# Kernel optimization log

Hardware: AMD Instinct MI355X
Metric: run time of the kernel (lower is better)

Reference implementation:

```python
import jax, jax.numpy as jnp
import numpy as np

THETA = 10.0      # neuron['theta']
TAU_SR = 10.0     # neuron['tauSr']
TAU_REF = 1.0     # neuron['tauRef']
SCALE_REF = 2.0   # neuron['scaleRef']
TAU_RHO = 1.0     # neuron['tauRho']
SCALE_RHO = 1.0   # neuron['scaleRho']
EPS = 0.01        # kernel truncation epsilon
TS = 1.0          # simulation['Ts']
T_SAMPLE = 256    # time steps == seq_len (forward sets tSample = embed_out.size(1))


def _alpha_kernel(tau, mult):
    # slayerPytorch _calculateAlphaKernel: mult * t/tau * exp(1 - t/tau), truncated
    ker = []
    for t in np.arange(0.0, T_SAMPLE * TS, TS):
        v = mult * t / tau * np.exp(1.0 - t / tau)
        if abs(v) < EPS and t > tau:
            break
        ker.append(v)
    return np.asarray(ker, dtype=np.float32)


def psp(x, srm_kernel):
    # Causal temporal filter: out[t] = Ts * sum_k srm[k] * x[t-k];  x: (B, C, T)
    B, C, T = x.shape
    K = srm_kernel.shape[0]
    lhs = x.reshape(B * C, 1, T)
    rhs = srm_kernel[::-1].reshape(1, 1, K)  # reverse: correlation -> convolution
    out = jax.lax.conv_general_dilated(lhs, rhs, (1,), [(K - 1, 0)])
    return out.reshape(B, C, T) * TS


def _spike_scan(u, ref_kernel):
    # Sequential threshold with refractory feedback (SLAYER getSpikes). u: (B, C, T)
    B, C, T = u.shape
    future = ref_kernel[1:]  # ref_kernel[0] == 0, so spike at t only affects t+1..
    R = future.shape[0]

    def step(r, u_t):
        m = u_t + r[..., 0]                       # membrane incl. past refractory
        s = (m >= THETA).astype(u.dtype)
        r = jnp.concatenate([r[..., 1:], jnp.zeros_like(r[..., :1])], axis=-1)
        r = r + s[..., None] * future             # schedule refractory response
        return r, (s, m)

    r0 = jnp.zeros((B, C, R), u.dtype)
    _, (s, m) = jax.lax.scan(step, r0, jnp.moveaxis(u, -1, 0))
    return jnp.moveaxis(s, 0, -1), jnp.moveaxis(m, 0, -1)


@jax.custom_vjp
def spike(u, ref_kernel):
    return _spike_scan(u, ref_kernel)[0]


def _spike_fwd(u, ref_kernel):
    s, m = _spike_scan(u, ref_kernel)
    return s, (m, ref_kernel)


def _spike_bwd(res, g):
    # SLAYER surrogate gradient: straight-through pdf on post-refractory membrane
    m, ref_kernel = res
    tau = TAU_RHO * THETA
    pdf = (SCALE_RHO / tau) * jnp.exp(-jnp.abs(m - THETA) / tau)
    return g * pdf, jnp.zeros_like(ref_kernel)


spike.defvjp(_spike_fwd, _spike_bwd)


def setup_inputs() -> dict:
    key = jax.random.key(0)
    k1, k2, k3, k4 = jax.random.split(key, 4)
    VOCAB, EMB, HID, OUT, B = 50000, 300, 512, 10, 64
    feed_data = jax.random.randint(k1, (B, T_SAMPLE), 0, VOCAB)
    emb_weight = jax.random.normal(k2, (VOCAB, EMB), jnp.float32)
    W1 = jax.random.normal(k3, (HID, EMB), jnp.float32) * (4.0 / np.sqrt(EMB))
    W2 = jax.random.normal(k4, (OUT, HID), jnp.float32) * (4.0 / np.sqrt(HID))
    return {
        "feed_data": feed_data,
        "emb_weight": emb_weight,
        "W1": W1,
        "W2": W2,
        "srm_kernel": jnp.asarray(_alpha_kernel(TAU_SR, 1.0)),
        "ref_kernel": jnp.asarray(_alpha_kernel(TAU_REF, -SCALE_REF * THETA)),
    }


def reference(feed_data, emb_weight, W1, W2, srm_kernel, ref_kernel):
    x = emb_weight[feed_data]                 # (B, T, E); dropout = identity (eval)
    x = jnp.transpose(x, (0, 2, 1))           # (B, E, T) -- transpose(1,2)
    h = jnp.einsum('he,bet->bht', W1, x)      # slayer.dense == 1x1x1 conv3d, no bias
    h = spike(psp(h, srm_kernel), ref_kernel)
    o = jnp.einsum('oh,bht->bot', W2, h)
    return spike(psp(o, srm_kernel), ref_kernel)  # (B, OUT, T)
```

## Files before the change

### kernel.cpp

```cpp
#include <hip/hip_runtime.h>

#define BB    64
#define TT    256
#define EMBD  300
#define HIDD  512
#define OUTC  10
#define THETA 10.0
#define FUTN  12
#define KSMAX 80
#define GT    32
#define GE    8
#define WGRP  9
#define WROW  (64 * WGRP)
#define HSTRD 258

__global__ __launch_bounds__(256)
void w2cvt_kernel(const float* __restrict__ W2, double* __restrict__ w2d)
{
    const int k = blockIdx.x * 256 + threadIdx.x;
    if (k < OUTC * HIDD) w2d[k] = (double)W2[k];
}

__global__ __launch_bounds__(512)
void gemm1_kernel(const int* __restrict__ feed, const float* __restrict__ emb,
                  const float* __restrict__ W1, double* __restrict__ m1)
{
    __shared__ double wl[GE * WROW];
    __shared__ double xs[GE][GT + 1];
    __shared__ int    idxb[GT];

    const int tid = threadIdx.x;
    const int t0  = blockIdx.x * GT;
    const int b   = blockIdx.y;

    if (tid < GT) idxb[tid] = feed[b * TT + t0 + tid];
    __syncthreads();

    const int cg = tid & 63;
    const int tg = tid >> 6;

    double acc[4][8];
#pragma unroll
    for (int i = 0; i < 4; ++i)
#pragma unroll
        for (int j = 0; j < 8; ++j) acc[i][j] = 0.0;

    const int NCH = (EMBD + GE - 1) / GE;
    for (int ch = 0; ch < NCH; ++ch) {
        const int e0 = ch * GE;
        {
            const int c = tid;
            float4 wa = make_float4(0.f, 0.f, 0.f, 0.f);
            float4 wb = make_float4(0.f, 0.f, 0.f, 0.f);
            if (e0 < EMBD)     wa = *(const float4*)&W1[(size_t)c * EMBD + e0];
            if (e0 + 4 < EMBD) wb = *(const float4*)&W1[(size_t)c * EMBD + e0 + 4];
            const int g = (c >> 3) * WGRP + (c & 7);
            wl[0 * WROW + g] = (double)wa.x;
            wl[1 * WROW + g] = (double)wa.y;
            wl[2 * WROW + g] = (double)wa.z;
            wl[3 * WROW + g] = (double)wa.w;
            wl[4 * WROW + g] = (double)wb.x;
            wl[5 * WROW + g] = (double)wb.y;
            wl[6 * WROW + g] = (double)wb.z;
            wl[7 * WROW + g] = (double)wb.w;
        }
        if (tid < 256) {
            const int t = tid >> 3, e = tid & 7;
            const float v = (e0 + e < EMBD)
                ? emb[(size_t)idxb[t] * EMBD + e0 + e] : 0.f;
            xs[e][t] = (double)v;
        }
        __syncthreads();

#pragma unroll
        for (int e = 0; e < GE; ++e) {
            const double* wp = &wl[e * WROW + cg * WGRP];
            const double w0 = wp[0], w1 = wp[1], w2 = wp[2], w3 = wp[3];
            const double w4 = wp[4], w5 = wp[5], w6 = wp[6], w7 = wp[7];
            const double x0 = xs[e][4 * tg + 0];
            const double x1 = xs[e][4 * tg + 1];
            const double x2 = xs[e][4 * tg + 2];
            const double x3 = xs[e][4 * tg + 3];
            acc[0][0] = fma(x0, w0, acc[0][0]); acc[0][1] = fma(x0, w1, acc[0][1]);
            acc[0][2] = fma(x0, w2, acc[0][2]); acc[0][3] = fma(x0, w3, acc[0][3]);
            acc[0][4] = fma(x0, w4, acc[0][4]); acc[0][5] = fma(x0, w5, acc[0][5]);
            acc[0][6] = fma(x0, w6, acc[0][6]); acc[0][7] = fma(x0, w7, acc[0][7]);
            acc[1][0] = fma(x1, w0, acc[1][0]); acc[1][1] = fma(x1, w1, acc[1][1]);
            acc[1][2] = fma(x1, w2, acc[1][2]); acc[1][3] = fma(x1, w3, acc[1][3]);
            acc[1][4] = fma(x1, w4, acc[1][4]); acc[1][5] = fma(x1, w5, acc[1][5]);
            acc[1][6] = fma(x1, w6, acc[1][6]); acc[1][7] = fma(x1, w7, acc[1][7]);
            acc[2][0] = fma(x2, w0, acc[2][0]); acc[2][1] = fma(x2, w1, acc[2][1]);
            acc[2][2] = fma(x2, w2, acc[2][2]); acc[2][3] = fma(x2, w3, acc[2][3]);
            acc[2][4] = fma(x2, w4, acc[2][4]); acc[2][5] = fma(x2, w5, acc[2][5]);
            acc[2][6] = fma(x2, w6, acc[2][6]); acc[2][7] = fma(x2, w7, acc[2][7]);
            acc[3][0] = fma(x3, w0, acc[3][0]); acc[3][1] = fma(x3, w1, acc[3][1]);
            acc[3][2] = fma(x3, w2, acc[3][2]); acc[3][3] = fma(x3, w3, acc[3][3]);
            acc[3][4] = fma(x3, w4, acc[3][4]); acc[3][5] = fma(x3, w5, acc[3][5]);
            acc[3][6] = fma(x3, w6, acc[3][6]); acc[3][7] = fma(x3, w7, acc[3][7]);
        }
        __syncthreads();
    }

#pragma unroll
    for (int i = 0; i < 4; ++i) {
        double* dst = &m1[((size_t)b * TT + t0 + 4 * tg + i) * HIDD + 8 * cg];
        *(double2*)(dst + 0) = make_double2(acc[i][0], acc[i][1]);
        *(double2*)(dst + 2) = make_double2(acc[i][2], acc[i][3]);
        *(double2*)(dst + 4) = make_double2(acc[i][4], acc[i][5]);
        *(double2*)(dst + 6) = make_double2(acc[i][6], acc[i][7]);
    }
}

__global__ __launch_bounds__(256)
void firscan_kernel(const double* __restrict__ m1, const float* __restrict__ srm,
                    const float* __restrict__ refk, unsigned char* __restrict__ s1,
                    int Ks, int Kr)
{
    __shared__ double        h[16 * HSTRD];
    __shared__ unsigned char sb[16 * 260];
    __shared__ double        srm_sm[KSMAX];

    const int tid = threadIdx.x;
    const int c0  = blockIdx.x * 16;
    const int b   = blockIdx.y;

    if (tid < KSMAX) srm_sm[tid] = (tid < Ks) ? (double)srm[tid] : 0.0;

    for (int u = tid; u < 16 * TT; u += 256) {
        const int c = u & 15, t = u >> 4;
        h[c * HSTRD + t] = m1[((size_t)b * TT + t) * HIDD + c0 + c];
    }
    __syncthreads();

    const int cf = tid & 15, tb = tid >> 4;
    const int t0 = tb * 16;
    const double* hrow = &h[cf * HSTRD];

    double pout[16];
#pragma unroll
    for (int k = 0; k < 16; ++k) pout[k] = 0.0;

    double HI[8], MID[8], LO[8];
#pragma unroll
    for (int k = 0; k < 8; ++k) {
        HI[k]  = hrow[t0 + 8 + k];
        MID[k] = hrow[t0 + k];
        const int idx = t0 - 8 + k;
        LO[k] = (idx >= 0) ? hrow[idx] : 0.0;
    }

#pragma unroll
    for (int jb = 0; jb < KSMAX; jb += 8) {
        double NEW[8];
        if (jb + 8 < KSMAX) {
#pragma unroll
            for (int k = 0; k < 8; ++k) {
                const int idx = t0 - jb - 16 + k;
                NEW[k] = (idx >= 0) ? hrow[idx] : 0.0;
            }
        }
#pragma unroll
        for (int jj = 0; jj < 8; ++jj) {
            const double sj = srm_sm[jb + jj];
#pragma unroll
            for (int i = 0; i < 16; ++i) {
                const int d = i - jj;
                const double hv = (d >= 8) ? HI[(d - 8) & 7]
                               : (d >= 0) ? MID[d & 7]
                                          : LO[(8 + d) & 7];
                pout[i] = fma(hv, sj, pout[i]);
            }
        }
        if (jb + 8 < KSMAX) {
#pragma unroll
            for (int k = 0; k < 8; ++k) { HI[k] = MID[k]; MID[k] = LO[k]; LO[k] = NEW[k]; }
        }
    }
    __syncthreads();
#pragma unroll
    for (int k = 0; k < 16; ++k)
        h[cf * HSTRD + t0 + k] = pout[k];
    __syncthreads();

    if (tid < 16) {
        double fut[FUTN], rsh[FUTN];
#pragma unroll
        for (int i = 0; i < FUTN; ++i) {
            fut[i] = (i + 1 < Kr) ? (double)refk[i + 1] : 0.0;
            rsh[i] = 0.0;
        }
        const double*  hr = &h[tid * HSTRD];
        unsigned char* sr = &sb[tid * 260];
        double un = hr[0];
        for (int t = 0; t < TT; ++t) {
            const double uc = un;
            un = (t < TT - 1) ? hr[t + 1] : 0.0;
            const double m  = uc + rsh[0];
            const double sv = (m >= THETA) ? 1.0 : 0.0;
#pragma unroll
            for (int i = 0; i < FUTN - 1; ++i) rsh[i] = fma(sv, fut[i], rsh[i + 1]);
            rsh[FUTN - 1] = sv * fut[FUTN - 1];
            sr[t] = (unsigned char)(sv != 0.0 ? 1 : 0);
        }
    }
    __syncthreads();

    {
        const int tl2 = tid & 63;
#pragma unroll
        for (int r = 0; r < 4; ++r) {
            const int c = (tid >> 6) + 4 * r;
            const unsigned int v = *(const unsigned int*)&sb[c * 260 + 4 * tl2];
            *(unsigned int*)&s1[((size_t)b * HIDD + c0 + c) * TT + 4 * tl2] = v;
        }
    }
}

__global__ __launch_bounds__(256, 2)
void layer2a_kernel(const unsigned char* __restrict__ s1,
                    const double* __restrict__ w2d, double* __restrict__ m2)
{
    __shared__ double w2l[OUTC * HIDD];
    __shared__ double red[4][OUTC][65];

    const int tid = threadIdx.x;
    const int b = blockIdx.x, q = blockIdx.y;
    const int tl = tid & 63, hq = tid >> 6;
    const int t  = q * 64 + tl;

    for (int u = tid; u < OUTC * HIDD; u += 256) w2l[u] = w2d[u];
    __syncthreads();

    double p[OUTC];
#pragma unroll
    for (int oc = 0; oc < OUTC; ++oc) p[oc] = 0.0;

    const unsigned char* sp = s1 + ((size_t)b * HIDD + hq * 128) * TT + t;
    for (int h0 = 0; h0 < 128; ++h0) {
        const double sv = (double)sp[(size_t)h0 * TT];
        const int hh = hq * 128 + h0;
#pragma unroll
        for (int oc = 0; oc < OUTC; ++oc)
            p[oc] = fma(sv, w2l[oc * HIDD + hh], p[oc]);
    }
#pragma unroll
    for (int oc = 0; oc < OUTC; ++oc) red[hq][oc][tl] = p[oc];
    __syncthreads();

    for (int u = tid; u < OUTC * 64; u += 256) {
        const int oc = u >> 6, t2 = u & 63;
        const double s = ((red[0][oc][t2] + red[1][oc][t2]) +
                          red[2][oc][t2]) + red[3][oc][t2];
        m2[((size_t)b * OUTC + oc) * TT + q * 64 + t2] = s;
    }
}

__global__ __launch_bounds__(256)
void layer2b_kernel(const double* __restrict__ m2, const float* __restrict__ srm,
                    const float* __restrict__ refk, float* __restrict__ out,
                    int Ks, int Kr)
{
    __shared__ double mh[OUTC][257];
    __shared__ double uh[OUTC][257];
    __shared__ double srm_sm[KSMAX];
    __shared__ unsigned char s2[OUTC][260];

    const int tid = threadIdx.x;
    const int b   = blockIdx.x;

    if (tid < KSMAX) srm_sm[tid] = (tid < Ks) ? (double)srm[tid] : 0.0;
    for (int u = tid; u < OUTC * TT; u += 256)
        mh[u >> 8][u & 255] = m2[(size_t)b * OUTC * TT + u];
    __syncthreads();

    double p[OUTC];
#pragma unroll
    for (int oc = 0; oc < OUTC; ++oc) p[oc] = 0.0;
    for (int j = 0; j < KSMAX; ++j) {
        const int idx = tid - j;
        if (idx >= 0) {
            const double sj = srm_sm[j];
#pragma unroll
            for (int oc = 0; oc < OUTC; ++oc)
                p[oc] = fma(mh[oc][idx], sj, p[oc]);
        }
    }
#pragma unroll
    for (int oc = 0; oc < OUTC; ++oc) uh[oc][tid] = p[oc];
    __syncthreads();

    if (tid < OUTC) {
        double fut[FUTN], rsh[FUTN];
#pragma unroll
        for (int i = 0; i < FUTN; ++i) {
            fut[i] = (i + 1 < Kr) ? (double)refk[i + 1] : 0.0;
            rsh[i] = 0.0;
        }
        for (int t = 0; t < TT; ++t) {
            const double m  = uh[tid][t] + rsh[0];
            const double sv = (m >= THETA) ? 1.0 : 0.0;
#pragma unroll
            for (int i = 0; i < FUTN - 1; ++i) rsh[i] = fma(sv, fut[i], rsh[i + 1]);
            rsh[FUTN - 1] = sv * fut[FUTN - 1];
            s2[tid][t] = (unsigned char)(sv != 0.0 ? 1 : 0);
        }
    }
    __syncthreads();

    for (int u = tid; u < OUTC * TT; u += 256)
        out[(size_t)b * OUTC * TT + u] = (float)s2[u >> 8][u & 255];
}

extern "C" void kernel_launch(void* const* d_in, const int* in_sizes, int n_in,
                              void* d_out, int out_size, void* d_ws, size_t ws_size,
                              hipStream_t stream)
{
    const int*   feed = (const int*)  d_in[0];
    const float* emb  = (const float*)d_in[1];
    const float* W1   = (const float*)d_in[2];
    const float* W2   = (const float*)d_in[3];
    const float* srm  = (const float*)d_in[4];
    const float* refk = (const float*)d_in[5];
    const int Ks = in_sizes[4];
    const int Kr = in_sizes[5];

    const size_t S1B  = (size_t)BB * HIDD * TT;
    const size_t W2DB = (size_t)OUTC * HIDD * 8;
    const size_t M2B  = (size_t)BB * OUTC * TT * 8;
    unsigned char* s1c = (unsigned char*)d_ws;
    double* w2d = (double*)((char*)d_ws + S1B);
    double* m2  = (double*)((char*)d_ws + S1B + W2DB);
    double* m1  = (double*)((char*)d_ws + S1B + W2DB + M2B);
    float*  out = (float*)d_out;

    w2cvt_kernel  <<<dim3(20),            256, 0, stream>>>(W2, w2d);
    gemm1_kernel  <<<dim3(TT / GT, BB),   512, 0, stream>>>(feed, emb, W1, m1);
    firscan_kernel<<<dim3(HIDD / 16, BB), 256, 0, stream>>>(m1, srm, refk, s1c, Ks, Kr);
    layer2a_kernel<<<dim3(BB, 4),         256, 0, stream>>>(s1c, w2d, m2);
    layer2b_kernel<<<dim3(BB),            256, 0, stream>>>(m2, srm, refk, out, Ks, Kr);
}
```

Before: 443.0 us.

## Split gemm1 across output-channel halves and prefetch next K-chunk into registers

```diff
diff --git a/kernel.cpp b/kernel.cpp
--- a/kernel.cpp
+++ b/kernel.cpp
@@ -9,9 +9,10 @@
 #define FUTN  12
 #define KSMAX 80
 #define GT    32
+#define GC    256
 #define GE    8
 #define WGRP  9
-#define WROW  (64 * WGRP)
+#define WROW  (32 * WGRP)
 #define HSTRD 258
 
 __global__ __launch_bounds__(256)
@@ -21,7 +22,7 @@
     if (k < OUTC * HIDD) w2d[k] = (double)W2[k];
 }
 
-__global__ __launch_bounds__(512)
+__global__ __launch_bounds__(256)
 void gemm1_kernel(const int* __restrict__ feed, const float* __restrict__ emb,
                   const float* __restrict__ W1, double* __restrict__ m1)
 {
@@ -30,14 +31,16 @@
     __shared__ int    idxb[GT];
 
     const int tid = threadIdx.x;
-    const int t0  = blockIdx.x * GT;
+    const int t0  = (blockIdx.x >> 1) * GT;
+    const int c0  = (blockIdx.x & 1) * GC;
     const int b   = blockIdx.y;
 
     if (tid < GT) idxb[tid] = feed[b * TT + t0 + tid];
     __syncthreads();
 
-    const int cg = tid & 63;
-    const int tg = tid >> 6;
+    const int cg = tid & 31;
+    const int tg = tid >> 5;
+    const int xt = tid >> 3, xe = tid & 7;
 
     double acc[4][8];
 #pragma unroll
@@ -45,32 +48,39 @@
 #pragma unroll
         for (int j = 0; j < 8; ++j) acc[i][j] = 0.0;
 
+    const size_t wrow = (size_t)(c0 + tid) * EMBD;
+    const size_t xrow = (size_t)idxb[xt] * EMBD;
+
+    float4 wa = make_float4(0.f, 0.f, 0.f, 0.f);
+    float4 wb = make_float4(0.f, 0.f, 0.f, 0.f);
+    float  xv = 0.f;
+    wa = *(const float4*)&W1[wrow + 0];
+    wb = *(const float4*)&W1[wrow + 4];
+    xv = emb[xrow + xe];
+
     const int NCH = (EMBD + GE - 1) / GE;
+    const int g   = (tid >> 3) * WGRP + (tid & 7);
+
     for (int ch = 0; ch < NCH; ++ch) {
-        const int e0 = ch * GE;
-        {
-            const int c = tid;
-            float4 wa = make_float4(0.f, 0.f, 0.f, 0.f);
-            float4 wb = make_float4(0.f, 0.f, 0.f, 0.f);
-            if (e0 < EMBD)     wa = *(const float4*)&W1[(size_t)c * EMBD + e0];
-            if (e0 + 4 < EMBD) wb = *(const float4*)&W1[(size_t)c * EMBD + e0 + 4];
-            const int g = (c >> 3) * WGRP + (c & 7);
-            wl[0 * WROW + g] = (double)wa.x;
-            wl[1 * WROW + g] = (double)wa.y;
-            wl[2 * WROW + g] = (double)wa.z;
-            wl[3 * WROW + g] = (double)wa.w;
-            wl[4 * WROW + g] = (double)wb.x;
-            wl[5 * WROW + g] = (double)wb.y;
-            wl[6 * WROW + g] = (double)wb.z;
-            wl[7 * WROW + g] = (double)wb.w;
-        }
-        if (tid < 256) {
-            const int t = tid >> 3, e = tid & 7;
-            const float v = (e0 + e < EMBD)
-                ? emb[(size_t)idxb[t] * EMBD + e0 + e] : 0.f;
-            xs[e][t] = (double)v;
-        }
+        wl[0 * WROW + g] = (double)wa.x;
+        wl[1 * WROW + g] = (double)wa.y;
+        wl[2 * WROW + g] = (double)wa.z;
+        wl[3 * WROW + g] = (double)wa.w;
+        wl[4 * WROW + g] = (double)wb.x;
+        wl[5 * WROW + g] = (double)wb.y;
+        wl[6 * WROW + g] = (double)wb.z;
+        wl[7 * WROW + g] = (double)wb.w;
+        xs[xe][xt] = (double)xv;
         __syncthreads();
+
+        if (ch + 1 < NCH) {
+            const int e0n = (ch + 1) * GE;
+            wa = make_float4(0.f, 0.f, 0.f, 0.f);
+            wb = make_float4(0.f, 0.f, 0.f, 0.f);
+            if (e0n < EMBD)     wa = *(const float4*)&W1[wrow + e0n];
+            if (e0n + 4 < EMBD) wb = *(const float4*)&W1[wrow + e0n + 4];
+            xv = (e0n + xe < EMBD) ? emb[xrow + e0n + xe] : 0.f;
+        }
 
 #pragma unroll
         for (int e = 0; e < GE; ++e) {
@@ -103,7 +113,7 @@
 
 #pragma unroll
     for (int i = 0; i < 4; ++i) {
-        double* dst = &m1[((size_t)b * TT + t0 + 4 * tg + i) * HIDD + 8 * cg];
+        double* dst = &m1[((size_t)b * TT + t0 + 4 * tg + i) * HIDD + c0 + 8 * cg];
         *(double2*)(dst + 0) = make_double2(acc[i][0], acc[i][1]);
         *(double2*)(dst + 2) = make_double2(acc[i][2], acc[i][3]);
         *(double2*)(dst + 4) = make_double2(acc[i][4], acc[i][5]);
@@ -333,9 +343,9 @@
     double* m1  = (double*)((char*)d_ws + S1B + W2DB + M2B);
     float*  out = (float*)d_out;
 
-    w2cvt_kernel  <<<dim3(20),            256, 0, stream>>>(W2, w2d);
-    gemm1_kernel  <<<dim3(TT / GT, BB),   512, 0, stream>>>(feed, emb, W1, m1);
-    firscan_kernel<<<dim3(HIDD / 16, BB), 256, 0, stream>>>(m1, srm, refk, s1c, Ks, Kr);
-    layer2a_kernel<<<dim3(BB, 4),         256, 0, stream>>>(s1c, w2d, m2);
-    layer2b_kernel<<<dim3(BB),            256, 0, stream>>>(m2, srm, refk, out, Ks, Kr);
-}
+    w2cvt_kernel  <<<dim3(20),                      256, 0, stream>>>(W2, w2d);
+    gemm1_kernel  <<<dim3((TT / GT) * (HIDD / GC), BB), 256, 0, stream>>>(feed, emb, W1, m1);
+    firscan_kernel<<<dim3(HIDD / 16, BB),           256, 0, stream>>>(m1, srm, refk, s1c, Ks, Kr);
+    layer2a_kernel<<<dim3(BB, 4),                   256, 0, stream>>>(s1c, w2d, m2);
+    layer2b_kernel<<<dim3(BB),                      256, 0, stream>>>(m2, srm, refk, out, Ks, Kr);
+}
```

Result: faster. 396.5 us (-10.5%).
